# Optimization experiments

Hardware: AMD Instinct MI355X
Metric: run time of the kernel (lower is better)

## Reference

```python
import jax, jax.numpy as jnp
import numpy as np

B, S, D, H = 4, 2048, 1024, 16
DEPTH = D // H
NEG = 1e10


def setup_inputs() -> dict:
    key = jax.random.key(0)
    ks = jax.random.split(key, 11)
    sc = 0.02
    return {
        "q": jax.random.normal(ks[0], (B, S, D), jnp.float32),
        "v": jax.random.normal(ks[1], (B, S, D), jnp.float32),
        "k": jax.random.normal(ks[2], (B, S, D), jnp.float32),
        "Wq": jax.random.normal(ks[3], (D, D), jnp.float32) * sc,
        "bq": jnp.zeros((D,), jnp.float32),
        "Wk": jax.random.normal(ks[4], (D, D), jnp.float32) * sc,
        "bk": jnp.zeros((D,), jnp.float32),
        "Wv": jax.random.normal(ks[5], (D, D), jnp.float32) * sc,
        "bv": jnp.zeros((D,), jnp.float32),
        "Wo": jax.random.normal(ks[6], (D, D), jnp.float32) * sc,
        "bo": jnp.zeros((D,), jnp.float32),
        "mask": 1,
    }


def _split_heads(x):
    # [B, S, D] -> [B, H, S, depth]
    b, s, _ = x.shape
    return x.reshape(b, s, H, DEPTH).transpose(0, 2, 1, 3)


def reference(q, v, k, Wq, bq, Wk, bk, Wv, bv, Wo, bo, mask):
    qh = _split_heads(q @ Wq + bq)
    kh = _split_heads(k @ Wk + bk)
    vh = _split_heads(v @ Wv + bv)

    scale = 1.0 / jnp.sqrt(jnp.asarray(DEPTH, jnp.float32))
    # [B, H, Sq, Sk]
    logits = jnp.einsum("bhqd,bhkd->bhqk", qh, kh) * scale

    if mask:
        nd, ns = logits.shape[-2], logits.shape[-1]
        i = jnp.arange(nd)[:, None]
        j = jnp.arange(ns)[None, :]
        b = (i >= j - ns + nd).astype(logits.dtype)  # lower triangle from lower-right
        logits = logits * b - NEG * (1.0 - b)

    attn = jax.nn.softmax(logits, axis=-1)
    out = jnp.einsum("bhqk,bhkd->bhqd", attn, vh)  # [B, H, Sq, depth]
    out = out.transpose(0, 2, 1, 3).reshape(q.shape[0], -1, D)  # concat heads
    return out @ Wo + bo
```

## Files before the change

### kernel.cpp

```cpp
#include <hip/hip_runtime.h>
#include <hip/hip_bf16.h>
#include <cstdint>
#include <cstddef>

#define S_LEN 2048
#define D_MODEL 1024
#define N_HEADS 16
#define DEPTH 64
#define BATCH 4

#define GLOBAL_AS __attribute__((address_space(1)))
#define LDS_AS __attribute__((address_space(3)))

typedef __attribute__((ext_vector_type(4))) float f32x4;
typedef __attribute__((ext_vector_type(8))) short bf16x8;
typedef __attribute__((ext_vector_type(4))) unsigned short us4;
typedef __attribute__((ext_vector_type(8))) unsigned short us8;

__device__ __forceinline__ unsigned short f2bf(float f) {
  unsigned int u = __builtin_bit_cast(unsigned int, f);
  u += 0x7FFFu + ((u >> 16) & 1u);
  return (unsigned short)(u >> 16);
}

__device__ __forceinline__ unsigned short f2bf_hw(float f) {
  return __builtin_bit_cast(unsigned short, __float2bfloat16(f));
}

struct TCArgs {
  const float* W[4];
  unsigned short* Wt[4];
  float scale[4];
};

__global__ __launch_bounds__(256) void transpose_cast4(TCArgs a, int N) {
  __shared__ float tile[32][33];
  int z = blockIdx.z;
  const float* W = a.W[z];
  unsigned short* Wt = a.Wt[z];
  float scale = a.scale[z];
  int bx = blockIdx.x * 32;
  int by = blockIdx.y * 32;
  int tx = threadIdx.x, ty = threadIdx.y;
#pragma unroll
  for (int i = 0; i < 4; ++i)
    tile[ty + i * 8][tx] = W[(size_t)(by + ty + i * 8) * N + bx + tx];
  __syncthreads();
#pragma unroll
  for (int i = 0; i < 4; ++i)
    Wt[(size_t)(bx + ty + i * 8) * N + by + tx] = f2bf(tile[tx][ty + i * 8] * scale);
}

__global__ __launch_bounds__(256) void transpose_v(const unsigned short* __restrict__ Vp,
                                                   unsigned short* __restrict__ Vt) {
  __shared__ unsigned short tile[64][72];
  int tid = threadIdx.x;
  int sb = blockIdx.x;
  int bh = blockIdx.y;
  int b = bh >> 4, h = bh & 15;
  int s0 = sb * 64;
#pragma unroll
  for (int rep = 0; rep < 2; ++rep) {
    int idx = rep * 256 + tid;
    int r = idx >> 3, c8 = idx & 7;
    us8 v = *(const us8*)(Vp + (size_t)(b * S_LEN + s0 + r) * D_MODEL + h * DEPTH + c8 * 8);
#pragma unroll
    for (int e = 0; e < 8; ++e) tile[c8 * 8 + e][r] = v[e];
  }
  __syncthreads();
#pragma unroll
  for (int rep = 0; rep < 2; ++rep) {
    int idx = rep * 256 + tid;
    int d = idx >> 3, c8 = idx & 7;
    us8 v = *(const us8*)&tile[d][c8 * 8];
    *(us8*)(Vt + ((size_t)(bh * DEPTH + d)) * S_LEN + s0 + c8 * 8) = v;
  }
}

struct GemmSlice {
  const void* A;
  const unsigned short* Bt;
  const float* bias;
  void* C;
  float bscale;
};
struct GemmArgs {
  GemmSlice s[3];
};

template <bool A_IS_F32, bool OUT_F32>
__global__ __launch_bounds__(256) void gemm_bt(GemmArgs args, int M, int N, int K) {
  constexpr int ASTR = A_IS_F32 ? 72 : 64;
  __shared__ unsigned short a_lds[128 * ASTR];
  __shared__ unsigned short b_lds[128 * 72];

  int slice = blockIdx.y >> 3;
  int nj = blockIdx.y & 7;
  const GemmSlice& g = args.s[slice];
  const float* Af = (const float*)g.A;
  const unsigned short* Ah = (const unsigned short*)g.A;
  const unsigned short* Bt = g.Bt;

  int tid = threadIdx.x;
  int wave = tid >> 6, lane = tid & 63;
  int l15 = lane & 15, lg = lane >> 4;
  int wm = wave >> 1, wn = wave & 1;

  int row0 = blockIdx.x * 128;
  int col0 = nj * 128;

  f32x4 acc[4][4] = {};
  f32x4 av[8];
  us8 bv[4];

  int ar = tid >> 4, ac4 = tid & 15;
  int br = tid >> 3, bc8 = tid & 7;

  auto loadA = [&](int k0) {
#pragma unroll
    for (int rep = 0; rep < 8; ++rep)
      av[rep] = *(const f32x4*)(Af + (size_t)(row0 + rep * 16 + ar) * K + k0 + ac4 * 4);
  };
  auto writeA = [&]() {
#pragma unroll
    for (int rep = 0; rep < 8; ++rep) {
      us4 h = {f2bf_hw(av[rep][0]), f2bf_hw(av[rep][1]),
               f2bf_hw(av[rep][2]), f2bf_hw(av[rep][3])};
      *(us4*)&a_lds[(rep * 16 + ar) * 72 + ac4 * 4] = h;
    }
  };
  auto loadB = [&](int k0) {
#pragma unroll
    for (int rep = 0; rep < 4; ++rep)
      bv[rep] = *(const us8*)(Bt + (size_t)(col0 + rep * 32 + br) * K + k0 + bc8 * 8);
  };
  auto writeB = [&]() {
#pragma unroll
    for (int rep = 0; rep < 4; ++rep)
      *(us8*)&b_lds[(rep * 32 + br) * 72 + bc8 * 8] = bv[rep];
  };
  auto issueA = [&](int k0) {
#pragma unroll
    for (int rep = 0; rep < 4; ++rep) {
      int chunk = (wave * 4 + rep) * 64 + lane;
      int row = chunk >> 3;
      int c8 = (chunk & 7) ^ (row & 7);
      __builtin_amdgcn_global_load_lds(
          (const GLOBAL_AS void*)(Ah + (size_t)(row0 + row) * K + k0 + c8 * 8),
          (LDS_AS void*)(&a_lds[chunk * 8]), 16, 0, 0);
    }
  };
  auto compute = [&]() {
#pragma unroll
    for (int kk = 0; kk < 2; ++kk) {
      bf16x8 af[4], bfr[4];
#pragma unroll
      for (int ii = 0; ii < 4; ++ii) {
        int row = wm * 64 + ii * 16 + l15;
        if constexpr (A_IS_F32)
          af[ii] = *(const bf16x8*)&a_lds[row * 72 + kk * 32 + lg * 8];
        else
          af[ii] = *(const bf16x8*)&a_lds[row * 64 + (((kk * 4 + lg) ^ (l15 & 7)) * 8)];
      }
#pragma unroll
      for (int jj = 0; jj < 4; ++jj) {
        int row = wn * 64 + jj * 16 + l15;
        bfr[jj] = *(const bf16x8*)&b_lds[row * 72 + kk * 32 + lg * 8];
      }
#pragma unroll
      for (int ii = 0; ii < 4; ++ii)
#pragma unroll
        for (int jj = 0; jj < 4; ++jj)
          acc[ii][jj] = __builtin_amdgcn_mfma_f32_16x16x32_bf16(af[ii], bfr[jj], acc[ii][jj], 0, 0, 0);
    }
  };

  int nk = K >> 6;
  loadB(0);
  if constexpr (A_IS_F32) loadA(0);

  for (int ki = 0; ki < nk; ++ki) {
    __syncthreads();
    writeB();
    if constexpr (A_IS_F32)
      writeA();
    else
      issueA(ki * 64);
    __syncthreads();
    if (ki + 1 < nk) {
      loadB((ki + 1) * 64);
      if constexpr (A_IS_F32) loadA((ki + 1) * 64);
    }
    compute();
  }

#pragma unroll
  for (int ii = 0; ii < 4; ++ii) {
#pragma unroll
    for (int jj = 0; jj < 4; ++jj) {
      int col = col0 + wn * 64 + jj * 16 + l15;
      float bv2 = g.bias[col] * g.bscale;
#pragma unroll
      for (int r = 0; r < 4; ++r) {
        int row = row0 + wm * 64 + ii * 16 + lg * 4 + r;
        float v = acc[ii][jj][r] + bv2;
        if constexpr (OUT_F32)
          ((float*)g.C)[(size_t)row * N + col] = v;
        else
          ((unsigned short*)g.C)[(size_t)row * N + col] = f2bf(v);
      }
    }
  }
}

__global__ __launch_bounds__(512) void attn_kernel(const unsigned short* __restrict__ Qp,
                                                   const unsigned short* __restrict__ Kp,
                                                   const unsigned short* __restrict__ Vt,
                                                   unsigned short* __restrict__ Op) {
  __shared__ unsigned short k_lds[64][76];
  __shared__ unsigned short vt_lds[64][76];
  __shared__ unsigned short p_lds[8][16][76];

  int tid = threadIdx.x;
  int w = tid >> 6, lane = tid & 63;
  int l15 = lane & 15, lg = lane >> 4;

  int bid = blockIdx.x;
  int swz = (bid & 7) * 64 + (bid >> 3);
  int pairIdx = swz & 7;
  int bh = swz >> 3;
  int b = bh >> 4, h = bh & 15;

  const unsigned short* Kbase = Kp + (size_t)b * S_LEN * D_MODEL + h * DEPTH;
  const unsigned short* Vbase = Vt + (size_t)bh * DEPTH * S_LEN;

  bool stageV = (tid >= 256);
  int st = tid & 255;
  int r = st >> 2, cb = (st & 3) * 16;
  const unsigned short* srow = stageV ? (Vbase + (size_t)r * S_LEN + cb)
                                      : (Kbase + (size_t)r * D_MODEL + cb);
  const size_t sstep = stageV ? 64 : (size_t)64 * D_MODEL;

  bf16x8 ones;
#pragma unroll
  for (int e = 0; e < 8; ++e) ones[e] = (short)0x3F80;

  for (int half = 0; half < 2; ++half) {
    int t = (half == 0) ? pairIdx : (15 - pairIdx);
    int q0 = t * 128;
    int nkv = 2 * t + 2;
    int q0w = q0 + w * 16;

    const unsigned short* qp =
        Qp + ((size_t)(b * S_LEN + q0 + w * 16 + l15)) * D_MODEL + h * DEPTH;
    bf16x8 qf0 = *(const bf16x8*)(qp + lg * 8);
    bf16x8 qf1 = *(const bf16x8*)(qp + 32 + lg * 8);

    f32x4 acc_l = (f32x4){0.f, 0.f, 0.f, 0.f};
    f32x4 acc_o[4];
#pragma unroll
    for (int dd = 0; dd < 4; ++dd) acc_o[dd] = (f32x4){0.f, 0.f, 0.f, 0.f};

    const unsigned short* sptr = srow;
    us8 s0 = *(const us8*)sptr;
    us8 s1 = *(const us8*)(sptr + 8);
    sptr += sstep;

    for (int kb = 0; kb < nkv; ++kb) {
      int k0 = kb * 64;
      __syncthreads();
      if (stageV) {
        *(us8*)&vt_lds[r][cb] = s0;
        *(us8*)&vt_lds[r][cb + 8] = s1;
      } else {
        *(us8*)&k_lds[r][cb] = s0;
        *(us8*)&k_lds[r][cb + 8] = s1;
      }
      __syncthreads();
      bool more = (kb + 1) < nkv;
      if (more) {
        s0 = *(const us8*)sptr;
        s1 = *(const us8*)(sptr + 8);
        sptr += sstep;
      }

      bool full_masked = (k0 > q0w + 15);
      if (!full_masked) {
        f32x4 s[4];
#pragma unroll
        for (int nf = 0; nf < 4; ++nf) s[nf] = (f32x4){0.f, 0.f, 0.f, 0.f};
        __builtin_amdgcn_s_setprio(1);
#pragma unroll
        for (int nf = 0; nf < 4; ++nf) {
          bf16x8 kf0 = *(const bf16x8*)&k_lds[nf * 16 + l15][lg * 8];
          bf16x8 kf1 = *(const bf16x8*)&k_lds[nf * 16 + l15][32 + lg * 8];
          s[nf] = __builtin_amdgcn_mfma_f32_16x16x32_bf16(qf0, kf0, s[nf], 0, 0, 0);
          s[nf] = __builtin_amdgcn_mfma_f32_16x16x32_bf16(qf1, kf1, s[nf], 0, 0, 0);
        }
        __builtin_amdgcn_s_setprio(0);

        bool diag = (k0 + 63 > q0w);
        if (diag) {
#pragma unroll
          for (int nf = 0; nf < 4; ++nf)
#pragma unroll
            for (int rr = 0; rr < 4; ++rr) {
              int qrow = q0w + lg * 4 + rr;
              int kcol = k0 + nf * 16 + l15;
              float x = (kcol > qrow) ? -1e10f : s[nf][rr];
              float p = __builtin_amdgcn_exp2f(x);
              p_lds[w][lg * 4 + rr][nf * 16 + l15] =
                  (unsigned short)(__builtin_bit_cast(unsigned int, p) >> 16);
            }
        } else {
#pragma unroll
          for (int nf = 0; nf < 4; ++nf)
#pragma unroll
            for (int rr = 0; rr < 4; ++rr) {
              float p = __builtin_amdgcn_exp2f(s[nf][rr]);
              p_lds[w][lg * 4 + rr][nf * 16 + l15] =
                  (unsigned short)(__builtin_bit_cast(unsigned int, p) >> 16);
            }
        }

        __builtin_amdgcn_s_setprio(1);
#pragma unroll
        for (int kk = 0; kk < 2; ++kk) {
          bf16x8 pf = *(const bf16x8*)&p_lds[w][l15][kk * 32 + lg * 8];
          acc_l = __builtin_amdgcn_mfma_f32_16x16x32_bf16(pf, ones, acc_l, 0, 0, 0);
#pragma unroll
          for (int dd = 0; dd < 4; ++dd) {
            bf16x8 vf = *(const bf16x8*)&vt_lds[dd * 16 + l15][kk * 32 + lg * 8];
            acc_o[dd] = __builtin_amdgcn_mfma_f32_16x16x32_bf16(pf, vf, acc_o[dd], 0, 0, 0);
          }
        }
        __builtin_amdgcn_s_setprio(0);
      }
    }

#pragma unroll
    for (int rr = 0; rr < 4; ++rr) {
      float inv = 1.0f / acc_l[rr];
      int qrow = q0 + w * 16 + lg * 4 + rr;
      unsigned short* op = Op + ((size_t)(b * S_LEN + qrow)) * D_MODEL + h * DEPTH;
#pragma unroll
      for (int dd = 0; dd < 4; ++dd)
        op[dd * 16 + l15] = f2bf(acc_o[dd][rr] * inv);
    }
  }
}

extern "C" void kernel_launch(void* const* d_in, const int* in_sizes, int n_in,
                              void* d_out, int out_size, void* d_ws, size_t ws_size,
                              hipStream_t stream) {
  const float* q  = (const float*)d_in[0];
  const float* v  = (const float*)d_in[1];
  const float* k  = (const float*)d_in[2];
  const float* Wq = (const float*)d_in[3];
  const float* bq = (const float*)d_in[4];
  const float* Wk = (const float*)d_in[5];
  const float* bk = (const float*)d_in[6];
  const float* Wv = (const float*)d_in[7];
  const float* bv = (const float*)d_in[8];
  const float* Wo = (const float*)d_in[9];
  const float* bo = (const float*)d_in[10];

  char* ws = (char*)d_ws;
  const size_t WSZ = (size_t)D_MODEL * D_MODEL * 2;
  const size_t XSZ = (size_t)BATCH * S_LEN * D_MODEL * 2;
  unsigned short* Wqt = (unsigned short*)(ws);
  unsigned short* Wkt = (unsigned short*)(ws + WSZ);
  unsigned short* Wvt = (unsigned short*)(ws + 2 * WSZ);
  unsigned short* Wot = (unsigned short*)(ws + 3 * WSZ);
  unsigned short* Qp  = (unsigned short*)(ws + 4 * WSZ);
  unsigned short* Kp  = (unsigned short*)(ws + 4 * WSZ + XSZ);
  unsigned short* Vp  = (unsigned short*)(ws + 4 * WSZ + 2 * XSZ);
  unsigned short* Vtp = (unsigned short*)(ws + 4 * WSZ + 3 * XSZ);
  unsigned short* AO  = Vp;

  const float SCL = 0.125f * 1.4426950408889634f;
  const int M = BATCH * S_LEN;

  TCArgs tc{};
  tc.W[0] = Wq;  tc.Wt[0] = Wqt;  tc.scale[0] = SCL;
  tc.W[1] = Wk;  tc.Wt[1] = Wkt;  tc.scale[1] = 1.0f;
  tc.W[2] = Wv;  tc.Wt[2] = Wvt;  tc.scale[2] = 1.0f;
  tc.W[3] = Wo;  tc.Wt[3] = Wot;  tc.scale[3] = 1.0f;
  hipLaunchKernelGGL(transpose_cast4, dim3(D_MODEL / 32, D_MODEL / 32, 4), dim3(32, 8),
                     0, stream, tc, D_MODEL);

  GemmArgs qkv{};
  qkv.s[0] = GemmSlice{(const void*)q, Wqt, bq, (void*)Qp, SCL};
  qkv.s[1] = GemmSlice{(const void*)k, Wkt, bk, (void*)Kp, 1.0f};
  qkv.s[2] = GemmSlice{(const void*)v, Wvt, bv, (void*)Vp, 1.0f};
  hipLaunchKernelGGL((gemm_bt<true, false>), dim3(M / 128, 24), dim3(256), 0, stream,
                     qkv, M, D_MODEL, D_MODEL);

  hipLaunchKernelGGL(transpose_v, dim3(S_LEN / 64, BATCH * N_HEADS), dim3(256), 0, stream,
                     Vp, Vtp);

  hipLaunchKernelGGL(attn_kernel, dim3(512), dim3(512), 0, stream, Qp, Kp, Vtp, AO);

  GemmArgs ao{};
  ao.s[0] = GemmSlice{(const void*)AO, Wot, bo, d_out, 1.0f};
  hipLaunchKernelGGL((gemm_bt<false, true>), dim3(M / 128, 8), dim3(256), 0, stream,
                     ao, M, D_MODEL, D_MODEL);
}
```

Before: 178.5 us.

## Give each attention wave two query tiles and drop async LDS loads in GEMM

The attention kernel goes from 8 waves with 16 query rows each to 4 waves with 32 rows each. Each K/V fragment read from LDS now feeds two MFMA row groups, and the staging loads become wider per thread. Separately, the bf16-A output GEMM drops global_load_lds with XOR swizzle in favour of register-staged loads into padded LDS rows (stride 76). The attention change trades occupancy and barrier granularity for better LDS reuse, and it raises register pressure.

```diff
diff --git a/kernel.cpp b/kernel.cpp
--- a/kernel.cpp
+++ b/kernel.cpp
@@ -8,9 +8,6 @@
 #define N_HEADS 16
 #define DEPTH 64
 #define BATCH 4
-
-#define GLOBAL_AS __attribute__((address_space(1)))
-#define LDS_AS __attribute__((address_space(3)))
 
 typedef __attribute__((ext_vector_type(4))) float f32x4;
 typedef __attribute__((ext_vector_type(8))) short bf16x8;
@@ -90,9 +87,10 @@
 
 template <bool A_IS_F32, bool OUT_F32>
 __global__ __launch_bounds__(256) void gemm_bt(GemmArgs args, int M, int N, int K) {
-  constexpr int ASTR = A_IS_F32 ? 72 : 64;
+  constexpr int ASTR = A_IS_F32 ? 72 : 76;
+  constexpr int BSTR = 76;
   __shared__ unsigned short a_lds[128 * ASTR];
-  __shared__ unsigned short b_lds[128 * 72];
+  __shared__ unsigned short b_lds[128 * BSTR];
 
   int slice = blockIdx.y >> 3;
   int nj = blockIdx.y & 7;
@@ -111,6 +109,7 @@
 
   f32x4 acc[4][4] = {};
   f32x4 av[8];
+  us8 avh[4];
   us8 bv[4];
 
   int ar = tid >> 4, ac4 = tid & 15;
@@ -129,6 +128,16 @@
       *(us4*)&a_lds[(rep * 16 + ar) * 72 + ac4 * 4] = h;
     }
   };
+  auto loadAh = [&](int k0) {
+#pragma unroll
+    for (int rep = 0; rep < 4; ++rep)
+      avh[rep] = *(const us8*)(Ah + (size_t)(row0 + rep * 32 + br) * K + k0 + bc8 * 8);
+  };
+  auto writeAh = [&]() {
+#pragma unroll
+    for (int rep = 0; rep < 4; ++rep)
+      *(us8*)&a_lds[(rep * 32 + br) * 76 + bc8 * 8] = avh[rep];
+  };
   auto loadB = [&](int k0) {
 #pragma unroll
     for (int rep = 0; rep < 4; ++rep)
@@ -137,18 +146,7 @@
   auto writeB = [&]() {
 #pragma unroll
     for (int rep = 0; rep < 4; ++rep)
-      *(us8*)&b_lds[(rep * 32 + br) * 72 + bc8 * 8] = bv[rep];
-  };
-  auto issueA = [&](int k0) {
-#pragma unroll
-    for (int rep = 0; rep < 4; ++rep) {
-      int chunk = (wave * 4 + rep) * 64 + lane;
-      int row = chunk >> 3;
-      int c8 = (chunk & 7) ^ (row & 7);
-      __builtin_amdgcn_global_load_lds(
-          (const GLOBAL_AS void*)(Ah + (size_t)(row0 + row) * K + k0 + c8 * 8),
-          (LDS_AS void*)(&a_lds[chunk * 8]), 16, 0, 0);
-    }
+      *(us8*)&b_lds[(rep * 32 + br) * BSTR + bc8 * 8] = bv[rep];
   };
   auto compute = [&]() {
 #pragma unroll
@@ -157,15 +155,12 @@
 #pragma unroll
       for (int ii = 0; ii < 4; ++ii) {
         int row = wm * 64 + ii * 16 + l15;
-        if constexpr (A_IS_F32)
-          af[ii] = *(const bf16x8*)&a_lds[row * 72 + kk * 32 + lg * 8];
-        else
-          af[ii] = *(const bf16x8*)&a_lds[row * 64 + (((kk * 4 + lg) ^ (l15 & 7)) * 8)];
+        af[ii] = *(const bf16x8*)&a_lds[row * ASTR + kk * 32 + lg * 8];
       }
 #pragma unroll
       for (int jj = 0; jj < 4; ++jj) {
         int row = wn * 64 + jj * 16 + l15;
-        bfr[jj] = *(const bf16x8*)&b_lds[row * 72 + kk * 32 + lg * 8];
+        bfr[jj] = *(const bf16x8*)&b_lds[row * BSTR + kk * 32 + lg * 8];
       }
 #pragma unroll
       for (int ii = 0; ii < 4; ++ii)
@@ -177,19 +172,16 @@
 
   int nk = K >> 6;
   loadB(0);
-  if constexpr (A_IS_F32) loadA(0);
+  if constexpr (A_IS_F32) loadA(0); else loadAh(0);
 
   for (int ki = 0; ki < nk; ++ki) {
     __syncthreads();
     writeB();
-    if constexpr (A_IS_F32)
-      writeA();
-    else
-      issueA(ki * 64);
+    if constexpr (A_IS_F32) writeA(); else writeAh();
     __syncthreads();
     if (ki + 1 < nk) {
       loadB((ki + 1) * 64);
-      if constexpr (A_IS_F32) loadA((ki + 1) * 64);
+      if constexpr (A_IS_F32) loadA((ki + 1) * 64); else loadAh((ki + 1) * 64);
     }
     compute();
   }
@@ -213,13 +205,13 @@
   }
 }
 
-__global__ __launch_bounds__(512) void attn_kernel(const unsigned short* __restrict__ Qp,
+__global__ __launch_bounds__(256) void attn_kernel(const unsigned short* __restrict__ Qp,
                                                    const unsigned short* __restrict__ Kp,
                                                    const unsigned short* __restrict__ Vt,
                                                    unsigned short* __restrict__ Op) {
   __shared__ unsigned short k_lds[64][76];
   __shared__ unsigned short vt_lds[64][76];
-  __shared__ unsigned short p_lds[8][16][76];
+  __shared__ unsigned short p_lds[4][32][76];
 
   int tid = threadIdx.x;
   int w = tid >> 6, lane = tid & 63;
@@ -234,9 +226,9 @@
   const unsigned short* Kbase = Kp + (size_t)b * S_LEN * D_MODEL + h * DEPTH;
   const unsigned short* Vbase = Vt + (size_t)bh * DEPTH * S_LEN;
 
-  bool stageV = (tid >= 256);
-  int st = tid & 255;
-  int r = st >> 2, cb = (st & 3) * 16;
+  bool stageV = (tid >= 128);
+  int st = tid & 127;
+  int r = st >> 1, cb = (st & 1) * 32;
   const unsigned short* srow = stageV ? (Vbase + (size_t)r * S_LEN + cb)
                                       : (Kbase + (size_t)r * D_MODEL + cb);
   const size_t sstep = stageV ? 64 : (size_t)64 * D_MODEL;
@@ -249,21 +241,29 @@
     int t = (half == 0) ? pairIdx : (15 - pairIdx);
     int q0 = t * 128;
     int nkv = 2 * t + 2;
-    int q0w = q0 + w * 16;
+    int qa0 = q0 + w * 32;
 
     const unsigned short* qp =
-        Qp + ((size_t)(b * S_LEN + q0 + w * 16 + l15)) * D_MODEL + h * DEPTH;
-    bf16x8 qf0 = *(const bf16x8*)(qp + lg * 8);
-    bf16x8 qf1 = *(const bf16x8*)(qp + 32 + lg * 8);
-
-    f32x4 acc_l = (f32x4){0.f, 0.f, 0.f, 0.f};
-    f32x4 acc_o[4];
-#pragma unroll
-    for (int dd = 0; dd < 4; ++dd) acc_o[dd] = (f32x4){0.f, 0.f, 0.f, 0.f};
+        Qp + ((size_t)(b * S_LEN + qa0 + l15)) * D_MODEL + h * DEPTH;
+    bf16x8 qa_0 = *(const bf16x8*)(qp + lg * 8);
+    bf16x8 qa_1 = *(const bf16x8*)(qp + 32 + lg * 8);
+    bf16x8 qb_0 = *(const bf16x8*)(qp + 16 * D_MODEL + lg * 8);
+    bf16x8 qb_1 = *(const bf16x8*)(qp + 16 * D_MODEL + 32 + lg * 8);
+
+    f32x4 acc_la = (f32x4){0.f, 0.f, 0.f, 0.f};
+    f32x4 acc_lb = (f32x4){0.f, 0.f, 0.f, 0.f};
+    f32x4 acc_oa[4], acc_ob[4];
+#pragma unroll
+    for (int dd = 0; dd < 4; ++dd) {
+      acc_oa[dd] = (f32x4){0.f, 0.f, 0.f, 0.f};
+      acc_ob[dd] = (f32x4){0.f, 0.f, 0.f, 0.f};
+    }
 
     const unsigned short* sptr = srow;
     us8 s0 = *(const us8*)sptr;
     us8 s1 = *(const us8*)(sptr + 8);
+    us8 s2 = *(const us8*)(sptr + 16);
+    us8 s3 = *(const us8*)(sptr + 24);
     sptr += sstep;
 
     for (int kb = 0; kb < nkv; ++kb) {
@@ -272,44 +272,58 @@
       if (stageV) {
         *(us8*)&vt_lds[r][cb] = s0;
         *(us8*)&vt_lds[r][cb + 8] = s1;
+        *(us8*)&vt_lds[r][cb + 16] = s2;
+        *(us8*)&vt_lds[r][cb + 24] = s3;
       } else {
         *(us8*)&k_lds[r][cb] = s0;
         *(us8*)&k_lds[r][cb + 8] = s1;
+        *(us8*)&k_lds[r][cb + 16] = s2;
+        *(us8*)&k_lds[r][cb + 24] = s3;
       }
       __syncthreads();
       bool more = (kb + 1) < nkv;
       if (more) {
         s0 = *(const us8*)sptr;
         s1 = *(const us8*)(sptr + 8);
+        s2 = *(const us8*)(sptr + 16);
+        s3 = *(const us8*)(sptr + 24);
         sptr += sstep;
       }
 
-      bool full_masked = (k0 > q0w + 15);
-      if (!full_masked) {
-        f32x4 s[4];
-#pragma unroll
-        for (int nf = 0; nf < 4; ++nf) s[nf] = (f32x4){0.f, 0.f, 0.f, 0.f};
+      bool doA = k0 <= qa0 + 15;
+      bool doB = k0 <= qa0 + 31;
+      if (doB) {
+        f32x4 sa[4], sb[4];
+#pragma unroll
+        for (int nf = 0; nf < 4; ++nf) {
+          sa[nf] = (f32x4){0.f, 0.f, 0.f, 0.f};
+          sb[nf] = (f32x4){0.f, 0.f, 0.f, 0.f};
+        }
         __builtin_amdgcn_s_setprio(1);
 #pragma unroll
         for (int nf = 0; nf < 4; ++nf) {
           bf16x8 kf0 = *(const bf16x8*)&k_lds[nf * 16 + l15][lg * 8];
           bf16x8 kf1 = *(const bf16x8*)&k_lds[nf * 16 + l15][32 + lg * 8];
-          s[nf] = __builtin_amdgcn_mfma_f32_16x16x32_bf16(qf0, kf0, s[nf], 0, 0, 0);
-          s[nf] = __builtin_amdgcn_mfma_f32_16x16x32_bf16(qf1, kf1, s[nf], 0, 0, 0);
+          sb[nf] = __builtin_amdgcn_mfma_f32_16x16x32_bf16(qb_0, kf0, sb[nf], 0, 0, 0);
+          sb[nf] = __builtin_amdgcn_mfma_f32_16x16x32_bf16(qb_1, kf1, sb[nf], 0, 0, 0);
+          if (doA) {
+            sa[nf] = __builtin_amdgcn_mfma_f32_16x16x32_bf16(qa_0, kf0, sa[nf], 0, 0, 0);
+            sa[nf] = __builtin_amdgcn_mfma_f32_16x16x32_bf16(qa_1, kf1, sa[nf], 0, 0, 0);
+          }
         }
         __builtin_amdgcn_s_setprio(0);
 
-        bool diag = (k0 + 63 > q0w);
-        if (diag) {
+        bool diagB = (k0 + 63 > qa0 + 16);
+        if (diagB) {
 #pragma unroll
           for (int nf = 0; nf < 4; ++nf)
 #pragma unroll
             for (int rr = 0; rr < 4; ++rr) {
-              int qrow = q0w + lg * 4 + rr;
+              int qrow = qa0 + 16 + lg * 4 + rr;
               int kcol = k0 + nf * 16 + l15;
-              float x = (kcol > qrow) ? -1e10f : s[nf][rr];
+              float x = (kcol > qrow) ? -1e10f : sb[nf][rr];
               float p = __builtin_amdgcn_exp2f(x);
-              p_lds[w][lg * 4 + rr][nf * 16 + l15] =
+              p_lds[w][16 + lg * 4 + rr][nf * 16 + l15] =
                   (unsigned short)(__builtin_bit_cast(unsigned int, p) >> 16);
             }
         } else {
@@ -317,21 +331,55 @@
           for (int nf = 0; nf < 4; ++nf)
 #pragma unroll
             for (int rr = 0; rr < 4; ++rr) {
-              float p = __builtin_amdgcn_exp2f(s[nf][rr]);
-              p_lds[w][lg * 4 + rr][nf * 16 + l15] =
+              float p = __builtin_amdgcn_exp2f(sb[nf][rr]);
+              p_lds[w][16 + lg * 4 + rr][nf * 16 + l15] =
                   (unsigned short)(__builtin_bit_cast(unsigned int, p) >> 16);
             }
         }
+        if (doA) {
+          bool diagA = (k0 + 63 > qa0);
+          if (diagA) {
+#pragma unroll
+            for (int nf = 0; nf < 4; ++nf)
+#pragma unroll
+              for (int rr = 0; rr < 4; ++rr) {
+                int qrow = qa0 + lg * 4 + rr;
+                int kcol = k0 + nf * 16 + l15;
+                float x = (kcol > qrow) ? -1e10f : sa[nf][rr];
+                float p = __builtin_amdgcn_exp2f(x);
+                p_lds[w][lg * 4 + rr][nf * 16 + l15] =
+                    (unsigned short)(__builtin_bit_cast(unsigned int, p) >> 16);
+              }
+          } else {
+#pragma unroll
+            for (int nf = 0; nf < 4; ++nf)
+#pragma unroll
+              for (int rr = 0; rr < 4; ++rr) {
+                float p = __builtin_amdgcn_exp2f(sa[nf][rr]);
+                p_lds[w][lg * 4 + rr][nf * 16 + l15] =
+                    (unsigned short)(__builtin_bit_cast(unsigned int, p) >> 16);
+              }
+          }
+        }
 
         __builtin_amdgcn_s_setprio(1);
 #pragma unroll
         for (int kk = 0; kk < 2; ++kk) {
-          bf16x8 pf = *(const bf16x8*)&p_lds[w][l15][kk * 32 + lg * 8];
-          acc_l = __builtin_amdgcn_mfma_f32_16x16x32_bf16(pf, ones, acc_l, 0, 0, 0);
-#pragma unroll
-          for (int dd = 0; dd < 4; ++dd) {
-            bf16x8 vf = *(const bf16x8*)&vt_lds[dd * 16 + l15][kk * 32 + lg * 8];
-            acc_o[dd] = __builtin_amdgcn_mfma_f32_16x16x32_bf16(pf, vf, acc_o[dd], 0, 0, 0);
+          bf16x8 vf[4];
+#pragma unroll
+          for (int dd = 0; dd < 4; ++dd)
+            vf[dd] = *(const bf16x8*)&vt_lds[dd * 16 + l15][kk * 32 + lg * 8];
+          bf16x8 pfb = *(const bf16x8*)&p_lds[w][16 + l15][kk * 32 + lg * 8];
+          acc_lb = __builtin_amdgcn_mfma_f32_16x16x32_bf16(pfb, ones, acc_lb, 0, 0, 0);
+#pragma unroll
+          for (int dd = 0; dd < 4; ++dd)
+            acc_ob[dd] = __builtin_amdgcn_mfma_f32_16x16x32_bf16(pfb, vf[dd], acc_ob[dd], 0, 0, 0);
+          if (doA) {
+            bf16x8 pfa = *(const bf16x8*)&p_lds[w][l15][kk * 32 + lg * 8];
+            acc_la = __builtin_amdgcn_mfma_f32_16x16x32_bf16(pfa, ones, acc_la, 0, 0, 0);
+#pragma unroll
+            for (int dd = 0; dd < 4; ++dd)
+              acc_oa[dd] = __builtin_amdgcn_mfma_f32_16x16x32_bf16(pfa, vf[dd], acc_oa[dd], 0, 0, 0);
           }
         }
         __builtin_amdgcn_s_setprio(0);
@@ -340,12 +388,16 @@
 
 #pragma unroll
     for (int rr = 0; rr < 4; ++rr) {
-      float inv = 1.0f / acc_l[rr];
-      int qrow = q0 + w * 16 + lg * 4 + rr;
-      unsigned short* op = Op + ((size_t)(b * S_LEN + qrow)) * D_MODEL + h * DEPTH;
-#pragma unroll
-      for (int dd = 0; dd < 4; ++dd)
-        op[dd * 16 + l15] = f2bf(acc_o[dd][rr] * inv);
+      float inva = 1.0f / acc_la[rr];
+      float invb = 1.0f / acc_lb[rr];
+      int qrowa = qa0 + lg * 4 + rr;
+      unsigned short* opa = Op + ((size_t)(b * S_LEN + qrowa)) * D_MODEL + h * DEPTH;
+      unsigned short* opb = opa + (size_t)16 * D_MODEL;
+#pragma unroll
+      for (int dd = 0; dd < 4; ++dd) {
+        opa[dd * 16 + l15] = f2bf(acc_oa[dd][rr] * inva);
+        opb[dd * 16 + l15] = f2bf(acc_ob[dd][rr] * invb);
+      }
     }
   }
 }
@@ -399,7 +451,7 @@
   hipLaunchKernelGGL(transpose_v, dim3(S_LEN / 64, BATCH * N_HEADS), dim3(256), 0, stream,
                      Vp, Vtp);
 
-  hipLaunchKernelGGL(attn_kernel, dim3(512), dim3(512), 0, stream, Qp, Kp, Vtp, AO);
+  hipLaunchKernelGGL(attn_kernel, dim3(512), dim3(256), 0, stream, Qp, Kp, Vtp, AO);
 
   GemmArgs ao{};
   ao.s[0] = GemmSlice{(const void*)AO, Wot, bo, d_out, 1.0f};
```

Measured after the change: 186.3 us. +4.4%, slower.

## Replace GEMMs with 256x128 double-buffered 8-wave kernel and pre-cast activations

Applied to the files above, without the earlier changes.

Adds a standalone kernel that casts q, k and v to bf16 up front, so every projection GEMM can read bf16 A tiles. The old 128x128 GEMM is replaced by a 512-thread kernel with 256x128 tiles and double-buffered global_load_lds staging for both A and B. That kernel interleaves quarter-tile MFMA groups with barriers, explicit vmcnt waits and setprio. The QKV projections now run as three separate launches with a block-index swizzle, and workspace buffers are aliased to fit the extra bf16 copies. This aims to overlap loads with compute and raise data reuse, at the cost of an extra full pass over the fp32 activations and a bank-conflict-prone unpadded LDS layout.

```diff
diff --git a/kernel.cpp b/kernel.cpp
--- a/kernel.cpp
+++ b/kernel.cpp
@@ -51,6 +51,29 @@
     Wt[(size_t)(bx + ty + i * 8) * N + by + tx] = f2bf(tile[tx][ty + i * 8] * scale);
 }
 
+__global__ __launch_bounds__(256) void cast3_bf16(const float* __restrict__ q,
+                                                  const float* __restrict__ k,
+                                                  const float* __restrict__ v,
+                                                  unsigned short* __restrict__ qb,
+                                                  unsigned short* __restrict__ kb,
+                                                  unsigned short* __restrict__ vb) {
+  size_t i = ((size_t)blockIdx.x * 256 + threadIdx.x) * 8;
+  f32x4 x0, x1;
+  us8 o;
+  x0 = *(const f32x4*)(q + i); x1 = *(const f32x4*)(q + i + 4);
+#pragma unroll
+  for (int e = 0; e < 4; ++e) { o[e] = f2bf_hw(x0[e]); o[e + 4] = f2bf_hw(x1[e]); }
+  *(us8*)(qb + i) = o;
+  x0 = *(const f32x4*)(k + i); x1 = *(const f32x4*)(k + i + 4);
+#pragma unroll
+  for (int e = 0; e < 4; ++e) { o[e] = f2bf_hw(x0[e]); o[e + 4] = f2bf_hw(x1[e]); }
+  *(us8*)(kb + i) = o;
+  x0 = *(const f32x4*)(v + i); x1 = *(const f32x4*)(v + i + 4);
+#pragma unroll
+  for (int e = 0; e < 4; ++e) { o[e] = f2bf_hw(x0[e]); o[e + 4] = f2bf_hw(x1[e]); }
+  *(us8*)(vb + i) = o;
+}
+
 __global__ __launch_bounds__(256) void transpose_v(const unsigned short* __restrict__ Vp,
                                                    unsigned short* __restrict__ Vt) {
   __shared__ unsigned short tile[64][72];
@@ -77,140 +100,140 @@
   }
 }
 
-struct GemmSlice {
-  const void* A;
-  const unsigned short* Bt;
-  const float* bias;
-  void* C;
-  float bscale;
-};
-struct GemmArgs {
-  GemmSlice s[3];
-};
-
-template <bool A_IS_F32, bool OUT_F32>
-__global__ __launch_bounds__(256) void gemm_bt(GemmArgs args, int M, int N, int K) {
-  constexpr int ASTR = A_IS_F32 ? 72 : 64;
-  __shared__ unsigned short a_lds[128 * ASTR];
-  __shared__ unsigned short b_lds[128 * 72];
-
-  int slice = blockIdx.y >> 3;
-  int nj = blockIdx.y & 7;
-  const GemmSlice& g = args.s[slice];
-  const float* Af = (const float*)g.A;
-  const unsigned short* Ah = (const unsigned short*)g.A;
-  const unsigned short* Bt = g.Bt;
-
-  int tid = threadIdx.x;
-  int wave = tid >> 6, lane = tid & 63;
-  int l15 = lane & 15, lg = lane >> 4;
-  int wm = wave >> 1, wn = wave & 1;
-
-  int row0 = blockIdx.x * 128;
-  int col0 = nj * 128;
+template <bool OUT_F32>
+__global__ __launch_bounds__(512) void gemm8(const unsigned short* __restrict__ A,
+                                             const unsigned short* __restrict__ Bt,
+                                             const float* __restrict__ bias,
+                                             float bscale,
+                                             void* __restrict__ Cptr,
+                                             int M, int N, int K) {
+  __shared__ unsigned short smem[49152];
+
+  const int tid = threadIdx.x;
+  const int wave = tid >> 6, lane = tid & 63;
+  const int l15 = lane & 15, lg = lane >> 4;
+  const int wm = wave >> 1, wn = wave & 1;
+
+  int bid = blockIdx.x;
+  int wk = ((bid & 7) << 5) | (bid >> 3);
+  int mi = wk >> 3, nj = wk & 7;
+  const int row0 = mi * 256, col0 = nj * 128;
+
+  const unsigned short* Ab = A + (size_t)row0 * K;
+  const unsigned short* Bb = Bt + (size_t)col0 * K;
 
   f32x4 acc[4][4] = {};
-  f32x4 av[8];
-  us8 bv[4];
-
-  int ar = tid >> 4, ac4 = tid & 15;
-  int br = tid >> 3, bc8 = tid & 7;
-
-  auto loadA = [&](int k0) {
-#pragma unroll
-    for (int rep = 0; rep < 8; ++rep)
-      av[rep] = *(const f32x4*)(Af + (size_t)(row0 + rep * 16 + ar) * K + k0 + ac4 * 4);
-  };
-  auto writeA = [&]() {
-#pragma unroll
-    for (int rep = 0; rep < 8; ++rep) {
-      us4 h = {f2bf_hw(av[rep][0]), f2bf_hw(av[rep][1]),
-               f2bf_hw(av[rep][2]), f2bf_hw(av[rep][3])};
-      *(us4*)&a_lds[(rep * 16 + ar) * 72 + ac4 * 4] = h;
+  bf16x8 aF[2][2];
+  bf16x8 bF[2][2][2];
+
+  const int nk = K >> 6;
+
+  auto bar = [&]() {
+    asm volatile("" ::: "memory");
+    __builtin_amdgcn_s_barrier();
+    asm volatile("" ::: "memory");
+  };
+  auto stageA = [&](int buf, int h, int t) {
+#pragma unroll
+    for (int j = 0; j < 2; ++j) {
+      int c = j * 512 + tid;
+      __builtin_amdgcn_global_load_lds(
+          (const GLOBAL_AS void*)(Ab + (size_t)(h * 128 + (c >> 3)) * K + t * 64 + (c & 7) * 8),
+          (LDS_AS void*)(&smem[buf * 24576 + h * 8192 + c * 8]), 16, 0, 0);
     }
   };
-  auto loadB = [&](int k0) {
-#pragma unroll
-    for (int rep = 0; rep < 4; ++rep)
-      bv[rep] = *(const us8*)(Bt + (size_t)(col0 + rep * 32 + br) * K + k0 + bc8 * 8);
-  };
-  auto writeB = [&]() {
-#pragma unroll
-    for (int rep = 0; rep < 4; ++rep)
-      *(us8*)&b_lds[(rep * 32 + br) * 72 + bc8 * 8] = bv[rep];
-  };
-  auto issueA = [&](int k0) {
-#pragma unroll
-    for (int rep = 0; rep < 4; ++rep) {
-      int chunk = (wave * 4 + rep) * 64 + lane;
-      int row = chunk >> 3;
-      int c8 = (chunk & 7) ^ (row & 7);
+  auto stageB = [&](int buf, int t) {
+#pragma unroll
+    for (int j = 0; j < 2; ++j) {
+      int c = j * 512 + tid;
       __builtin_amdgcn_global_load_lds(
-          (const GLOBAL_AS void*)(Ah + (size_t)(row0 + row) * K + k0 + c8 * 8),
-          (LDS_AS void*)(&a_lds[chunk * 8]), 16, 0, 0);
+          (const GLOBAL_AS void*)(Bb + (size_t)(c >> 3) * K + t * 64 + (c & 7) * 8),
+          (LDS_AS void*)(&smem[buf * 24576 + 16384 + c * 8]), 16, 0, 0);
     }
   };
-  auto compute = [&]() {
-#pragma unroll
-    for (int kk = 0; kk < 2; ++kk) {
-      bf16x8 af[4], bfr[4];
-#pragma unroll
-      for (int ii = 0; ii < 4; ++ii) {
-        int row = wm * 64 + ii * 16 + l15;
-        if constexpr (A_IS_F32)
-          af[ii] = *(const bf16x8*)&a_lds[row * 72 + kk * 32 + lg * 8];
+  auto readA = [&](int buf, int a) {
+#pragma unroll
+    for (int mfi = 0; mfi < 2; ++mfi)
+#pragma unroll
+      for (int kk = 0; kk < 2; ++kk) {
+        int row = wm * 64 + (a * 2 + mfi) * 16 + l15;
+        aF[mfi][kk] = *(const bf16x8*)&smem[buf * 24576 + row * 64 + kk * 32 + lg * 8];
+      }
+  };
+  auto readB = [&](int buf, int b) {
+#pragma unroll
+    for (int nfi = 0; nfi < 2; ++nfi)
+#pragma unroll
+      for (int kk = 0; kk < 2; ++kk) {
+        int row = wn * 64 + (b * 2 + nfi) * 16 + l15;
+        bF[b][nfi][kk] = *(const bf16x8*)&smem[buf * 24576 + 16384 + row * 64 + kk * 32 + lg * 8];
+      }
+  };
+  auto quad = [&](int a, int b) {
+    __builtin_amdgcn_s_setprio(1);
+#pragma unroll
+    for (int mfi = 0; mfi < 2; ++mfi)
+#pragma unroll
+      for (int nfi = 0; nfi < 2; ++nfi)
+#pragma unroll
+        for (int kk = 0; kk < 2; ++kk)
+          acc[a * 2 + mfi][b * 2 + nfi] = __builtin_amdgcn_mfma_f32_16x16x32_bf16(
+              aF[mfi][kk], bF[b][nfi][kk], acc[a * 2 + mfi][b * 2 + nfi], 0, 0, 0);
+    __builtin_amdgcn_s_setprio(0);
+  };
+
+  stageB(0, 0);
+  stageA(0, 0, 0);
+  stageA(0, 1, 0);
+  stageB(1, 1);
+  asm volatile("s_waitcnt vmcnt(2)" ::: "memory");
+  bar();
+
+  for (int i2 = 0; i2 < nk / 2; ++i2) {
+    int t0 = 2 * i2, t1 = t0 + 1;
+    bool s2 = (t0 + 2) < nk, s3 = (t1 + 2) < nk;
+    readA(0, 0); readB(0, 0);
+    stageA(1, 0, t1);
+    bar(); quad(0, 0); bar();
+    readB(0, 1);
+    stageA(1, 1, t1);
+    bar(); quad(0, 1); bar();
+    readA(0, 1);
+    if (s2) stageB(0, t0 + 2);
+    bar(); quad(1, 0); bar();
+    if (s2) stageA(0, 0, t0 + 2);
+    bar(); quad(1, 1);
+    asm volatile("s_waitcnt vmcnt(4)" ::: "memory");
+    bar();
+    readA(1, 0); readB(1, 0);
+    if (s2) stageA(0, 1, t0 + 2);
+    bar(); quad(0, 0); bar();
+    readB(1, 1);
+    bar(); quad(0, 1); bar();
+    readA(1, 1);
+    if (s3) stageB(1, t1 + 2);
+    bar(); quad(1, 0); bar();
+    quad(1, 1);
+    asm volatile("s_waitcnt vmcnt(2)" ::: "memory");
+    bar();
+  }
+
+#pragma unroll
+  for (int mf = 0; mf < 4; ++mf)
+#pragma unroll
+    for (int nf = 0; nf < 4; ++nf) {
+      int col = col0 + wn * 64 + nf * 16 + l15;
+      float bv = bias[col] * bscale;
+#pragma unroll
+      for (int r = 0; r < 4; ++r) {
+        int row = row0 + wm * 64 + mf * 16 + lg * 4 + r;
+        float v = acc[mf][nf][r] + bv;
+        if constexpr (OUT_F32)
+          ((float*)Cptr)[(size_t)row * N + col] = v;
         else
-          af[ii] = *(const bf16x8*)&a_lds[row * 64 + (((kk * 4 + lg) ^ (l15 & 7)) * 8)];
-      }
-#pragma unroll
-      for (int jj = 0; jj < 4; ++jj) {
-        int row = wn * 64 + jj * 16 + l15;
-        bfr[jj] = *(const bf16x8*)&b_lds[row * 72 + kk * 32 + lg * 8];
-      }
-#pragma unroll
-      for (int ii = 0; ii < 4; ++ii)
-#pragma unroll
-        for (int jj = 0; jj < 4; ++jj)
-          acc[ii][jj] = __builtin_amdgcn_mfma_f32_16x16x32_bf16(af[ii], bfr[jj], acc[ii][jj], 0, 0, 0);
+          ((unsigned short*)Cptr)[(size_t)row * N + col] = f2bf(v);
+      }
     }
-  };
-
-  int nk = K >> 6;
-  loadB(0);
-  if constexpr (A_IS_F32) loadA(0);
-
-  for (int ki = 0; ki < nk; ++ki) {
-    __syncthreads();
-    writeB();
-    if constexpr (A_IS_F32)
-      writeA();
-    else
-      issueA(ki * 64);
-    __syncthreads();
-    if (ki + 1 < nk) {
-      loadB((ki + 1) * 64);
-      if constexpr (A_IS_F32) loadA((ki + 1) * 64);
-    }
-    compute();
-  }
-
-#pragma unroll
-  for (int ii = 0; ii < 4; ++ii) {
-#pragma unroll
-    for (int jj = 0; jj < 4; ++jj) {
-      int col = col0 + wn * 64 + jj * 16 + l15;
-      float bv2 = g.bias[col] * g.bscale;
-#pragma unroll
-      for (int r = 0; r < 4; ++r) {
-        int row = row0 + wm * 64 + ii * 16 + lg * 4 + r;
-        float v = acc[ii][jj][r] + bv2;
-        if constexpr (OUT_F32)
-          ((float*)g.C)[(size_t)row * N + col] = v;
-        else
-          ((unsigned short*)g.C)[(size_t)row * N + col] = f2bf(v);
-      }
-    }
-  }
 }
 
 __global__ __launch_bounds__(512) void attn_kernel(const unsigned short* __restrict__ Qp,
@@ -372,11 +395,15 @@
   unsigned short* Wkt = (unsigned short*)(ws + WSZ);
   unsigned short* Wvt = (unsigned short*)(ws + 2 * WSZ);
   unsigned short* Wot = (unsigned short*)(ws + 3 * WSZ);
-  unsigned short* Qp  = (unsigned short*)(ws + 4 * WSZ);
-  unsigned short* Kp  = (unsigned short*)(ws + 4 * WSZ + XSZ);
-  unsigned short* Vp  = (unsigned short*)(ws + 4 * WSZ + 2 * XSZ);
-  unsigned short* Vtp = (unsigned short*)(ws + 4 * WSZ + 3 * XSZ);
-  unsigned short* AO  = Vp;
+  char* act = ws + 4 * WSZ;
+  unsigned short* qb  = (unsigned short*)(act);
+  unsigned short* kb  = (unsigned short*)(act + XSZ);
+  unsigned short* vb  = (unsigned short*)(act + 2 * XSZ);
+  unsigned short* Qp  = (unsigned short*)(act + 3 * XSZ);
+  unsigned short* Kp  = qb;
+  unsigned short* Vp  = kb;
+  unsigned short* Vtp = vb;
+  unsigned short* AO  = kb;
 
   const float SCL = 0.125f * 1.4426950408889634f;
   const int M = BATCH * S_LEN;
@@ -389,20 +416,20 @@
   hipLaunchKernelGGL(transpose_cast4, dim3(D_MODEL / 32, D_MODEL / 32, 4), dim3(32, 8),
                      0, stream, tc, D_MODEL);
 
-  GemmArgs qkv{};
-  qkv.s[0] = GemmSlice{(const void*)q, Wqt, bq, (void*)Qp, SCL};
-  qkv.s[1] = GemmSlice{(const void*)k, Wkt, bk, (void*)Kp, 1.0f};
-  qkv.s[2] = GemmSlice{(const void*)v, Wvt, bv, (void*)Vp, 1.0f};
-  hipLaunchKernelGGL((gemm_bt<true, false>), dim3(M / 128, 24), dim3(256), 0, stream,
-                     qkv, M, D_MODEL, D_MODEL);
+  hipLaunchKernelGGL(cast3_bf16, dim3(4096), dim3(256), 0, stream, q, k, v, qb, kb, vb);
+
+  hipLaunchKernelGGL((gemm8<false>), dim3(256), dim3(512), 0, stream,
+                     qb, Wqt, bq, SCL, (void*)Qp, M, D_MODEL, D_MODEL);
+  hipLaunchKernelGGL((gemm8<false>), dim3(256), dim3(512), 0, stream,
+                     kb, Wkt, bk, 1.0f, (void*)Kp, M, D_MODEL, D_MODEL);
+  hipLaunchKernelGGL((gemm8<false>), dim3(256), dim3(512), 0, stream,
+                     vb, Wvt, bv, 1.0f, (void*)Vp, M, D_MODEL, D_MODEL);
 
   hipLaunchKernelGGL(transpose_v, dim3(S_LEN / 64, BATCH * N_HEADS), dim3(256), 0, stream,
                      Vp, Vtp);
 
   hipLaunchKernelGGL(attn_kernel, dim3(512), dim3(512), 0, stream, Qp, Kp, Vtp, AO);
 
-  GemmArgs ao{};
-  ao.s[0] = GemmSlice{(const void*)AO, Wot, bo, d_out, 1.0f};
-  hipLaunchKernelGGL((gemm_bt<false, true>), dim3(M / 128, 8), dim3(256), 0, stream,
-                     ao, M, D_MODEL, D_MODEL);
-}
+  hipLaunchKernelGGL((gemm8<true>), dim3(256), dim3(512), 0, stream,
+                     AO, Wot, bo, 1.0f, d_out, M, D_MODEL, D_MODEL);
+}
```

New measurement: 217.5 us. 1.22x slower.
